# Kernel tuning notes

Hardware: AMD Instinct MI355X
Metric: run time of the kernel (lower is better)

Reference implementation:

```python
import jax, jax.numpy as jnp
import numpy as np

B, N = 64, 1500
F_MIN, F_MAX = 0.5, 3.0  # HR band in Hz (30-180 bpm)
SAMPLING_F = 0.002       # frequency grid step -> F = 1251 frequencies
FS = 30.0                # video frame rate


def setup_inputs() -> dict:
    key = jax.random.key(0)
    k1, k2 = jax.random.split(key)
    x = jax.random.normal(k1, (B, N), dtype=jnp.float32)
    # true frequencies inside the searched band
    f_true = jax.random.uniform(k2, (B,), dtype=jnp.float32, minval=F_MIN, maxval=F_MAX)
    fs = jnp.full((B,), FS, dtype=jnp.float32)
    deltas = jnp.zeros((B,), dtype=jnp.float32)  # accepted but unused by the loss
    return {
        "x": x,
        "f_true": f_true,
        "fs": fs,
        "deltas": deltas,
        "sampling_f": SAMPLING_F,
        "f_range": (F_MIN, F_MAX),
    }


def reference(x, f_true, fs, deltas, sampling_f, f_range):
    f_min, f_max = f_range
    # frequency grid, same semantics as torch.arange(f_min, f_max+step, step)
    f_values = jnp.arange(f_min, f_max + sampling_f, sampling_f, dtype=jnp.float32)  # [F]
    n = jnp.arange(x.shape[1], dtype=jnp.float32)  # [N] time indices
    # angles[b,f,n] = 2*pi * f_values[f] * n / fs[b]  (fs varies per sample)
    phase = (2.0 * jnp.pi) * (f_values[None, :, None] * n[None, None, :]) / fs[:, None, None]  # [B,F,N]
    # PSD at each grid frequency: (sum x cos)^2 + (sum x sin)^2, batched as one contraction
    cos_terms = jnp.einsum('bn,bfn->bf', x, jnp.cos(phase))  # [B,F]
    sin_terms = jnp.einsum('bn,bfn->bf', x, jnp.sin(phase))  # [B,F]
    psd = cos_terms ** 2 + sin_terms ** 2                    # [B,F]
    log_lik = jnp.log(jax.nn.softmax(psd, axis=1) + 1e-8)    # [B,F]
    # index of grid frequency closest to f_true (non-differentiable gather index)
    idx = jnp.argmin(jnp.abs(f_values[None, :] - f_true[:, None]), axis=1)  # [B]
    per_sample = -jnp.take_along_axis(log_lik, idx[:, None], axis=1)[:, 0]  # [B]
    return jnp.mean(per_sample)
```

## Files before the change

kernel.cpp:

```cpp
#include <hip/hip_runtime.h>

#define BATCH 64
#define NSAMP 1500
#define NFREQ 1251
#define NSEG  5
#define SEGLEN 300
#define FBLK  256
#define FCHUNKS 5

__global__ __launch_bounds__(256) void goertzel_kernel(
    const float* __restrict__ x,
    const float* __restrict__ fs,
    const float* __restrict__ sampling_f,
    const float* __restrict__ f_range,
    float2* __restrict__ pcs,
    float* __restrict__ out)
{
    __shared__ float4 xs4[SEGLEN / 4];
    const int b   = blockIdx.x;
    const int seg = blockIdx.z;
    const int tid = threadIdx.x;
    const int n0  = seg * SEGLEN;

    if (b == 0 && seg == 0 && blockIdx.y == 0 && tid == 0) out[0] = 0.0f;

    const float4* xg = reinterpret_cast<const float4*>(x + b * NSAMP + n0);
    for (int i = tid; i < SEGLEN / 4; i += FBLK) xs4[i] = xg[i];
    __syncthreads();

    const int fidx = blockIdx.y * FBLK + tid;
    if (fidx >= NFREQ) return;

    const float f_min = f_range[0];
    const float step  = sampling_f[0];
    const float delta = (f_min + step) - f_min;
    const float fv    = f_min + (float)fidx * delta;

    const float rho = fv / fs[b];
    float rf = rho - floorf(rho);
    const float coef = 2.0f * __builtin_amdgcn_cosf(rf);

    float s1 = 0.0f, s2 = 0.0f;
#pragma unroll 5
    for (int k = 0; k < SEGLEN / 4; ++k) {
        float4 v = xs4[k];
        float t;
        t = fmaf(coef, s1, v.x - s2); s2 = s1; s1 = t;
        t = fmaf(coef, s1, v.y - s2); s2 = s1; s1 = t;
        t = fmaf(coef, s1, v.z - s2); s2 = s1; s1 = t;
        t = fmaf(coef, s1, v.w - s2); s2 = s1; s1 = t;
    }

    float aM  = (float)SEGLEN * rho;        aM  -= floorf(aM);
    float aM1 = (float)(SEGLEN - 1) * rho;  aM1 -= floorf(aM1);
    float a0  = (float)n0 * rho;            a0  -= floorf(a0);
    const float cM  = __builtin_amdgcn_cosf(aM);
    const float sM  = __builtin_amdgcn_sinf(aM);
    const float cM1 = __builtin_amdgcn_cosf(aM1);
    const float sM1 = __builtin_amdgcn_sinf(aM1);
    const float c0  = __builtin_amdgcn_cosf(a0);
    const float s0  = __builtin_amdgcn_sinf(a0);

    const float Cl = cM1 * s1 - cM * s2;
    const float Sl = sM1 * s1 - sM * s2;
    const float C  = c0 * Cl - s0 * Sl;
    const float S  = s0 * Cl + c0 * Sl;

    pcs[(b * NSEG + seg) * NFREQ + fidx] = make_float2(C, S);
}

__global__ __launch_bounds__(256) void loss_kernel(
    const float2* __restrict__ pcs,
    const float* __restrict__ f_true,
    const float* __restrict__ sampling_f,
    const float* __restrict__ f_range,
    float* __restrict__ out)
{
    const int b    = blockIdx.x;
    const int tid  = threadIdx.x;
    const int wave = tid >> 6;
    const int lane = tid & 63;

    __shared__ float wm[4];
    __shared__ float wl[4];
    __shared__ float s_pidx;

    const float f_min = f_range[0];
    const float step  = sampling_f[0];
    const float delta = (f_min + step) - f_min;
    const float ft    = f_true[b];

    int iq = (int)((ft - f_min) / delta + 0.5f);
    int lo = iq - 2; if (lo < 0) lo = 0;
    int hi = iq + 2; if (hi > NFREQ - 1) hi = NFREQ - 1;
    int   idx   = lo;
    float bestd = fabsf((f_min + (float)lo * delta) - ft);
    for (int i = lo + 1; i <= hi; ++i) {
        float d = fabsf((f_min + (float)i * delta) - ft);
        if (d < bestd) { bestd = d; idx = i; }
    }

    float m = -INFINITY, l = 0.0f;
    for (int i = tid; i < NFREQ; i += 256) {
        float c = 0.0f, s = 0.0f;
#pragma unroll
        for (int g = 0; g < NSEG; ++g) {
            float2 v = pcs[(b * NSEG + g) * NFREQ + i];
            c += v.x; s += v.y;
        }
        float v = fmaf(c, c, s * s);
        if (i == idx) s_pidx = v;
        float mn = fmaxf(m, v);
        l = l * __expf(m - mn) + __expf(v - mn);
        m = mn;
    }
    for (int off = 32; off > 0; off >>= 1) {
        float m2 = __shfl_down(m, off);
        float l2 = __shfl_down(l, off);
        float mn = fmaxf(m, m2);
        l = l * __expf(m - mn) + l2 * __expf(m2 - mn);
        m = mn;
    }
    if (lane == 0) { wm[wave] = m; wl[wave] = l; }
    __syncthreads();

    if (tid == 0) {
        float gm = wm[0], gl = wl[0];
#pragma unroll
        for (int w = 1; w < 4; ++w) {
            float mn = fmaxf(gm, wm[w]);
            gl = gl * __expf(gm - mn) + wl[w] * __expf(wm[w] - mn);
            gm = mn;
        }
        float sm  = __expf(s_pidx - gm) / gl;
        float per = -logf(sm + 1e-8f);
        atomicAdd(out, per * (1.0f / (float)BATCH));
    }
}

extern "C" void kernel_launch(void* const* d_in, const int* in_sizes, int n_in,
                              void* d_out, int out_size, void* d_ws, size_t ws_size,
                              hipStream_t stream) {
    const float* x          = (const float*)d_in[0];
    const float* f_true     = (const float*)d_in[1];
    const float* fs         = (const float*)d_in[2];
    const float* sampling_f = (const float*)d_in[4];
    const float* f_range    = (const float*)d_in[5];

    float2* pcs = (float2*)d_ws;

    dim3 g1(BATCH, FCHUNKS, NSEG);
    goertzel_kernel<<<g1, FBLK, 0, stream>>>(x, fs, sampling_f, f_range, pcs,
                                             (float*)d_out);
    loss_kernel<<<BATCH, 256, 0, stream>>>(pcs, f_true, sampling_f, f_range,
                                           (float*)d_out);
}
```

Baseline: 75.20 us.

## Compute five frequencies per thread in Goertzel kernel to reuse shared inputs

Each thread now runs five independent Goertzel recurrences over different frequencies, and the frequency-chunk grid dimension is removed. This reuses each shared-memory sample load across five chains and exposes instruction-level parallelism within a thread. The trade-off is a five-times smaller grid, which lowers occupancy and worsens load balance across CUs. The division by fs is also replaced by a reciprocal multiply.

```diff
diff --git a/kernel.cpp b/kernel.cpp
--- a/kernel.cpp
+++ b/kernel.cpp
@@ -6,7 +6,7 @@
 #define NSEG  5
 #define SEGLEN 300
 #define FBLK  256
-#define FCHUNKS 5
+#define FPT   5
 
 __global__ __launch_bounds__(256) void goertzel_kernel(
     const float* __restrict__ x,
@@ -18,55 +18,65 @@
 {
     __shared__ float4 xs4[SEGLEN / 4];
     const int b   = blockIdx.x;
-    const int seg = blockIdx.z;
+    const int seg = blockIdx.y;
     const int tid = threadIdx.x;
     const int n0  = seg * SEGLEN;
 
-    if (b == 0 && seg == 0 && blockIdx.y == 0 && tid == 0) out[0] = 0.0f;
+    if (b == 0 && seg == 0 && tid == 0) out[0] = 0.0f;
 
     const float4* xg = reinterpret_cast<const float4*>(x + b * NSAMP + n0);
     for (int i = tid; i < SEGLEN / 4; i += FBLK) xs4[i] = xg[i];
     __syncthreads();
 
-    const int fidx = blockIdx.y * FBLK + tid;
-    if (fidx >= NFREQ) return;
-
     const float f_min = f_range[0];
     const float step  = sampling_f[0];
     const float delta = (f_min + step) - f_min;
-    const float fv    = f_min + (float)fidx * delta;
+    const float inv_fs = 1.0f / fs[b];
 
-    const float rho = fv / fs[b];
-    float rf = rho - floorf(rho);
-    const float coef = 2.0f * __builtin_amdgcn_cosf(rf);
+    float coef[FPT], s1[FPT], s2[FPT], rho[FPT];
+#pragma unroll
+    for (int j = 0; j < FPT; ++j) {
+        const int fidx = j * FBLK + tid;
+        const float fv = f_min + (float)fidx * delta;
+        rho[j] = fv * inv_fs;
+        float rf = rho[j] - floorf(rho[j]);
+        coef[j] = 2.0f * __builtin_amdgcn_cosf(rf);
+        s1[j] = 0.0f; s2[j] = 0.0f;
+    }
 
-    float s1 = 0.0f, s2 = 0.0f;
-#pragma unroll 5
     for (int k = 0; k < SEGLEN / 4; ++k) {
         float4 v = xs4[k];
-        float t;
-        t = fmaf(coef, s1, v.x - s2); s2 = s1; s1 = t;
-        t = fmaf(coef, s1, v.y - s2); s2 = s1; s1 = t;
-        t = fmaf(coef, s1, v.z - s2); s2 = s1; s1 = t;
-        t = fmaf(coef, s1, v.w - s2); s2 = s1; s1 = t;
+#pragma unroll
+        for (int j = 0; j < FPT; ++j) {
+            float t;
+            t = fmaf(coef[j], s1[j], v.x - s2[j]); s2[j] = s1[j]; s1[j] = t;
+            t = fmaf(coef[j], s1[j], v.y - s2[j]); s2[j] = s1[j]; s1[j] = t;
+            t = fmaf(coef[j], s1[j], v.z - s2[j]); s2[j] = s1[j]; s1[j] = t;
+            t = fmaf(coef[j], s1[j], v.w - s2[j]); s2[j] = s1[j]; s1[j] = t;
+        }
     }
 
-    float aM  = (float)SEGLEN * rho;        aM  -= floorf(aM);
-    float aM1 = (float)(SEGLEN - 1) * rho;  aM1 -= floorf(aM1);
-    float a0  = (float)n0 * rho;            a0  -= floorf(a0);
-    const float cM  = __builtin_amdgcn_cosf(aM);
-    const float sM  = __builtin_amdgcn_sinf(aM);
-    const float cM1 = __builtin_amdgcn_cosf(aM1);
-    const float sM1 = __builtin_amdgcn_sinf(aM1);
-    const float c0  = __builtin_amdgcn_cosf(a0);
-    const float s0  = __builtin_amdgcn_sinf(a0);
+    float2* row = pcs + (b * NSEG + seg) * NFREQ;
+#pragma unroll
+    for (int j = 0; j < FPT; ++j) {
+        const int fidx = j * FBLK + tid;
+        float aM  = (float)SEGLEN * rho[j];        aM  -= floorf(aM);
+        float aM1 = (float)(SEGLEN - 1) * rho[j];  aM1 -= floorf(aM1);
+        float a0  = (float)n0 * rho[j];            a0  -= floorf(a0);
+        const float cM  = __builtin_amdgcn_cosf(aM);
+        const float sM  = __builtin_amdgcn_sinf(aM);
+        const float cM1 = __builtin_amdgcn_cosf(aM1);
+        const float sM1 = __builtin_amdgcn_sinf(aM1);
+        const float c0  = __builtin_amdgcn_cosf(a0);
+        const float s0  = __builtin_amdgcn_sinf(a0);
 
-    const float Cl = cM1 * s1 - cM * s2;
-    const float Sl = sM1 * s1 - sM * s2;
-    const float C  = c0 * Cl - s0 * Sl;
-    const float S  = s0 * Cl + c0 * Sl;
+        const float Cl = cM1 * s1[j] - cM * s2[j];
+        const float Sl = sM1 * s1[j] - sM * s2[j];
+        const float C  = c0 * Cl - s0 * Sl;
+        const float S  = s0 * Cl + c0 * Sl;
 
-    pcs[(b * NSEG + seg) * NFREQ + fidx] = make_float2(C, S);
+        if (fidx < NFREQ) row[fidx] = make_float2(C, S);
+    }
 }
 
 __global__ __launch_bounds__(256) void loss_kernel(
@@ -149,7 +159,7 @@
 
     float2* pcs = (float2*)d_ws;
 
-    dim3 g1(BATCH, FCHUNKS, NSEG);
+    dim3 g1(BATCH, NSEG);
     goertzel_kernel<<<g1, FBLK, 0, stream>>>(x, fs, sampling_f, f_range, pcs,
                                              (float*)d_out);
     loss_kernel<<<BATCH, 256, 0, stream>>>(pcs, f_true, sampling_f, f_range,
```

Measured after the change: 76.92 us. +2.3%, slower.
